# Kernel optimization log

Hardware: AMD Instinct MI355X
Metric: run time of the kernel (lower is better)

## Reference

```python
import jax, jax.numpy as jnp
import numpy as np

B, S, D, H, E = 8, 196, 768, 12, 8
HD = D // H  # 64
FF = 4 * D   # 3072
EPS = 1e-5


def setup_inputs() -> dict:
    key = jax.random.key(0)
    ks = jax.random.split(key, 12)
    s = 0.02
    inp = {
        'x': jax.random.normal(ks[0], (B, S, D), jnp.float32),
        'ln1_g': jnp.ones((D,), jnp.float32),
        'ln1_b': jnp.zeros((D,), jnp.float32),
        'Wq': jax.random.normal(ks[1], (D, D), jnp.float32) * s,
        'bq': jnp.zeros((D,), jnp.float32),
        'Wk': jax.random.normal(ks[2], (D, HD), jnp.float32) * s,
        'bk': jnp.zeros((HD,), jnp.float32),
        'Wv': jax.random.normal(ks[3], (D, HD), jnp.float32) * s,
        'bv': jnp.zeros((HD,), jnp.float32),
        'ln2_g': jnp.ones((D,), jnp.float32),
        'ln2_b': jnp.zeros((D,), jnp.float32),
        'Wg': jax.random.normal(ks[4], (D, E), jnp.float32) * s,
        'bg': jnp.zeros((E,), jnp.float32),
        'W1': jax.random.normal(ks[5], (E, D, FF), jnp.float32) * s,
        'b1': jnp.zeros((E, FF), jnp.float32),
        'W2': jax.random.normal(ks[6], (E, FF, D), jnp.float32) * s,
        'b2': jnp.zeros((E, D), jnp.float32),
    }
    return inp


def _layernorm(x, g, b):
    mu = jnp.mean(x, axis=-1, keepdims=True)
    var = jnp.var(x, axis=-1, keepdims=True)
    return (x - mu) * jax.lax.rsqrt(var + EPS) * g + b


def _rotate_half(x):
    x1, x2 = jnp.split(x, 2, axis=-1)
    return jnp.concatenate((-x2, x1), axis=-1)


def _rope(seq_len):
    inv_freq = 1.0 / (10000.0 ** (jnp.arange(0, HD, 2, dtype=jnp.float32) / HD))
    freqs = jnp.arange(seq_len, dtype=jnp.float32)[:, None] * inv_freq[None, :]
    emb = jnp.concatenate((freqs, freqs), axis=-1)  # [S, HD]
    return emb[None, :, None, :]  # [1, S, 1, HD]


def _attention(x, Wq, bq, Wk, bk, Wv, bv):
    b, s, _ = x.shape
    q = (x @ Wq + bq).reshape(b, s, H, HD)
    k = (x @ Wk + bk).reshape(b, s, 1, HD)
    v = (x @ Wv + bv).reshape(b, s, 1, HD)
    k = jnp.broadcast_to(k, (b, s, H, HD))
    v = jnp.broadcast_to(v, (b, s, H, HD))
    pe = _rope(s)
    cos, sin = jnp.cos(pe), jnp.sin(pe)
    q = q * cos + _rotate_half(q) * sin
    k = k * cos + _rotate_half(k) * sin
    scale = HD ** -0.5
    # NOTE: faithful to source -- matmul over the last two dims of [b,s,h,d],
    # i.e. attention across HEADS, not sequence positions.
    attn = jnp.einsum('bshd,bsgd->bshg', q, k) * scale
    attn = jax.nn.softmax(attn, axis=-1)
    out = jnp.einsum('bshg,bsgd->bshd', attn, v)
    return out.reshape(b, s, H * HD)


def _moe(x, Wg, bg, W1, b1, W2, b2):
    b, s, d = x.shape
    xt = x.reshape(-1, d)  # [T, D]
    gates = jax.nn.softmax(xt @ Wg + bg, axis=-1)
    top1 = jnp.argmax(gates, axis=-1)  # topk(k=2)[:,0] == argmax
    out = jnp.zeros_like(xt)
    for e in range(E):  # small fixed expert count
        h = jax.nn.gelu(xt @ W1[e] + b1[e], approximate=False)
        y = h @ W2[e] + b2[e]
        out = jnp.where((top1 == e)[:, None], y, out)
    return out.reshape(b, s, d)


def reference(x, ln1_g, ln1_b, Wq, bq, Wk, bk, Wv, bv, ln2_g, ln2_b, Wg, bg, W1, b1, W2, b2):
    res = x
    h = _layernorm(x, ln1_g, ln1_b)
    h = _attention(h, Wq, bq, Wk, bk, Wv, bv)
    x = res + h
    res = x
    h = _layernorm(x, ln2_g, ln2_b)
    h = _moe(h, Wg, bg, W1, b1, W2, b2)
    return res + h
```

## Files before the change

### kernel.cpp

```cpp
#include <hip/hip_runtime.h>


typedef unsigned short u16;
typedef short bf16x8_t __attribute__((ext_vector_type(8)));
typedef short bf16x4_t __attribute__((ext_vector_type(4)));
typedef float f32x4_t  __attribute__((ext_vector_type(4)));

#define T_TOK 1568
#define DM 768
#define HD 64
#define FF 3072
#define NE 8
#define LDSW 44

#define OFF_CNT   0
#define OFF_N12   32
#define OFF_ITEM1 64
#define OFF_ITEM2 864
#define OFF_BUCK  4096
#define OFF_H2    54272
#define OFF_HMID  2462720

__device__ __forceinline__ float bf2f(u16 h) {
    unsigned u = ((unsigned)h) << 16;
    return __builtin_bit_cast(float, u);
}
__device__ __forceinline__ u16 f2bf(float f) {
    unsigned u = __builtin_bit_cast(unsigned, f);
    unsigned r = (u + 0x7FFFu + ((u >> 16) & 1u)) >> 16;
    return (u16)r;
}
__device__ __forceinline__ float gelu_f(float x) {
    return 0.5f * x * (1.0f + erff(x * 0.70710678118654752440f));
}

__global__ __launch_bounds__(256) void k_pre(
        const float* __restrict__ x,
        const float* __restrict__ g1, const float* __restrict__ b1,
        const float* __restrict__ Wv, const float* __restrict__ bv,
        const float* __restrict__ g2, const float* __restrict__ b2g,
        const float* __restrict__ Wg, const float* __restrict__ bg,
        const float* __restrict__ b2moe,
        u16* __restrict__ h2, float* __restrict__ out,
        int* __restrict__ cnt, int* __restrict__ buck) {
    __shared__ __align__(16) u16 h1s[8 * DM];
    __shared__ float wgs[NE * DM];
    __shared__ float g2s[DM], b2s[DM];
    __shared__ float ps[4 * 8 * 64];
    __shared__ float vsm[8 * 64];
    int tid = threadIdx.x, lane = tid & 63, w = tid >> 6;
    int tb = blockIdx.x * 8;

    for (int idx = tid; idx < NE * DM; idx += 256) {
        int e = idx / DM, c = idx % DM;
        wgs[idx] = Wg[(size_t)c * NE + e];
    }
    for (int idx = tid; idx < DM; idx += 256) { g2s[idx] = g2[idx]; b2s[idx] = b2g[idx]; }

    float xv[2][12];
#pragma unroll
    for (int ttl = 0; ttl < 2; ttl++) {
        int tl = w * 2 + ttl;
        int t = tb + tl;
        const float* xp = x + (size_t)t * DM;
        float s = 0.0f;
#pragma unroll
        for (int i = 0; i < 12; i++) { float q = xp[lane + 64 * i]; xv[ttl][i] = q; s += q; }
#pragma unroll
        for (int m = 1; m < 64; m <<= 1) s += __shfl_xor(s, m);
        float mu = s * (1.0f / DM);
        float vs = 0.0f;
#pragma unroll
        for (int i = 0; i < 12; i++) { float d = xv[ttl][i] - mu; vs += d * d; }
#pragma unroll
        for (int m = 1; m < 64; m <<= 1) vs += __shfl_xor(vs, m);
        float rs = rsqrtf(vs * (1.0f / DM) + 1e-5f);
#pragma unroll
        for (int i = 0; i < 12; i++) {
            int c = lane + 64 * i;
            h1s[tl * DM + c] = f2bf((xv[ttl][i] - mu) * rs * g1[c] + b1[c]);
        }
    }
    __syncthreads();

    float acc[8];
#pragma unroll
    for (int tt = 0; tt < 8; tt++) acc[tt] = 0.0f;
    const float* wp = Wv + (size_t)(w * 192) * HD + lane;
    for (int kk = 0; kk < 192; kk += 4) {
        float w0 = wp[(size_t)(kk + 0) * HD];
        float w1 = wp[(size_t)(kk + 1) * HD];
        float w2 = wp[(size_t)(kk + 2) * HD];
        float w3 = wp[(size_t)(kk + 3) * HD];
        int kb = w * 192 + kk;
#pragma unroll
        for (int tt = 0; tt < 8; tt++) {
            bf16x4_t hh = *(const bf16x4_t*)&h1s[tt * DM + kb];
            acc[tt] += bf2f((u16)hh[0]) * w0 + bf2f((u16)hh[1]) * w1 +
                       bf2f((u16)hh[2]) * w2 + bf2f((u16)hh[3]) * w3;
        }
    }
#pragma unroll
    for (int tt = 0; tt < 8; tt++) ps[(w * 8 + tt) * 64 + lane] = acc[tt];
    __syncthreads();
#pragma unroll
    for (int s2 = 0; s2 < 2; s2++) {
        int tt = w * 2 + s2;
        vsm[tt * 64 + lane] = ps[tt * 64 + lane] + ps[(8 + tt) * 64 + lane] +
                              ps[(16 + tt) * 64 + lane] + ps[(24 + tt) * 64 + lane] +
                              bv[lane];
    }
    __syncthreads();

#pragma unroll
    for (int ttl = 0; ttl < 2; ttl++) {
        int tl = w * 2 + ttl;
        int t = tb + tl;
        float vl = vsm[tl * 64 + lane];
        float x2v[12];
        float s = 0.0f;
#pragma unroll
        for (int i = 0; i < 12; i++) { float q = xv[ttl][i] + vl; x2v[i] = q; s += q; }
#pragma unroll
        for (int m = 1; m < 64; m <<= 1) s += __shfl_xor(s, m);
        float mu = s * (1.0f / DM);
        float vs = 0.0f;
#pragma unroll
        for (int i = 0; i < 12; i++) { float d = x2v[i] - mu; vs += d * d; }
#pragma unroll
        for (int m = 1; m < 64; m <<= 1) vs += __shfl_xor(vs, m);
        float rs = rsqrtf(vs * (1.0f / DM) + 1e-5f);
        float le[NE];
#pragma unroll
        for (int e = 0; e < NE; e++) le[e] = 0.0f;
        u16* h2p = h2 + (size_t)t * DM;
#pragma unroll
        for (int i = 0; i < 12; i++) {
            int c = lane + 64 * i;
            float h = (x2v[i] - mu) * rs * g2s[c] + b2s[c];
            h2p[c] = f2bf(h);
#pragma unroll
            for (int e = 0; e < NE; e++) le[e] += h * wgs[e * DM + c];
        }
#pragma unroll
        for (int e = 0; e < NE; e++) {
#pragma unroll
            for (int m = 1; m < 64; m <<= 1) le[e] += __shfl_xor(le[e], m);
        }
        float best = le[0] + bg[0]; int be = 0;
#pragma unroll
        for (int e = 1; e < NE; e++) {
            float q = le[e] + bg[e];
            if (q > best) { best = q; be = e; }
        }
        if (lane == 0) {
            int pos = atomicAdd(&cnt[be], 1);
            buck[be * T_TOK + pos] = t;
        }
        float* op = out + (size_t)t * DM;
        const float* bp = b2moe + (size_t)be * DM;
#pragma unroll
        for (int i = 0; i < 12; i++) {
            int c = lane + 64 * i;
            op[c] = x2v[i] + bp[c];
        }
    }
}

__global__ void k_plan(const int* __restrict__ cnt, int* __restrict__ n12,
                       int* __restrict__ item1, int* __restrict__ item2) {
    if (threadIdx.x == 0) {
        int n1 = 0, n2 = 0;
        for (int e = 0; e < NE; e++) {
            int mts = (cnt[e] + 127) >> 7;
            for (int mt = 0; mt < mts; mt++) {
                int code = e * 64 + mt;
                item1[n1++] = code;
                for (int kc = 0; kc < 4; kc++) item2[n2++] = code * 4 + kc;
            }
        }
        n12[0] = n1; n12[1] = n2;
    }
}

__global__ __launch_bounds__(256) void k_moe_gemm1(
        const u16* __restrict__ h2, const float* __restrict__ W1,
        const float* __restrict__ b1, const int* __restrict__ cnt,
        const int* __restrict__ n12, const int* __restrict__ item1,
        const int* __restrict__ buck, u16* __restrict__ hmid) {
    int nt = blockIdx.x, n0 = nt * 128;
    int n1 = n12[0];
    int tid = threadIdx.x, lane = tid & 63, wid = tid >> 6;
    int arow = tid >> 2, ac = tid & 3;
    int bn = tid & 127, bkg = tid >> 7;
    int lr = lane & 15, q = lane >> 4;
    __shared__ __align__(16) u16 As[128 * LDSW];
    __shared__ __align__(16) u16 Bs[128 * LDSW];

    for (int it = blockIdx.y; it < n1; it += gridDim.y) {
        int code = item1[it];
        int e = code >> 6, mt = code & 63;
        int cnte = cnt[e], m0 = mt * 128;
        const float* W1e = W1 + (size_t)e * DM * FF;
        int atok[2];
#pragma unroll
        for (int j = 0; j < 2; j++) {
            int i = m0 + arow + 64 * j;
            atok[j] = (i < cnte) ? buck[e * T_TOK + i] : -1;
        }
        f32x4_t acc[2][8];
#pragma unroll
        for (int mi = 0; mi < 2; mi++)
#pragma unroll
            for (int ni = 0; ni < 8; ni++) acc[mi][ni] = (f32x4_t){0.f, 0.f, 0.f, 0.f};

        bf16x8_t a_pre[2];
        float b_pre[16];
#pragma unroll
        for (int j = 0; j < 2; j++) {
            bf16x8_t v = {0, 0, 0, 0, 0, 0, 0, 0};
            if (atok[j] >= 0) v = *(const bf16x8_t*)&h2[(size_t)atok[j] * DM + ac * 8];
            a_pre[j] = v;
        }
        {
            const float* bp = W1e + (size_t)(bkg * 16) * FF + n0 + bn;
#pragma unroll
            for (int kk = 0; kk < 16; kk++) b_pre[kk] = bp[(size_t)kk * FF];
        }
        const int NK = DM / 32;
        for (int kt = 0; kt < NK; kt++) {
            __syncthreads();
#pragma unroll
            for (int j = 0; j < 2; j++)
                *(bf16x8_t*)&As[(arow + 64 * j) * LDSW + ac * 8] = a_pre[j];
            {
                bf16x8_t p0, p1;
#pragma unroll
                for (int kk = 0; kk < 8; kk++) {
                    p0[kk] = (short)f2bf(b_pre[kk]);
                    p1[kk] = (short)f2bf(b_pre[kk + 8]);
                }
                *(bf16x8_t*)&Bs[bn * LDSW + bkg * 16] = p0;
                *(bf16x8_t*)&Bs[bn * LDSW + bkg * 16 + 8] = p1;
            }
            __syncthreads();
            if (kt + 1 < NK) {
                int k0 = (kt + 1) * 32;
#pragma unroll
                for (int j = 0; j < 2; j++) {
                    bf16x8_t v = {0, 0, 0, 0, 0, 0, 0, 0};
                    if (atok[j] >= 0)
                        v = *(const bf16x8_t*)&h2[(size_t)atok[j] * DM + k0 + ac * 8];
                    a_pre[j] = v;
                }
                const float* bp = W1e + (size_t)(k0 + bkg * 16) * FF + n0 + bn;
#pragma unroll
                for (int kk = 0; kk < 16; kk++) b_pre[kk] = bp[(size_t)kk * FF];
            }
            bf16x8_t af[2];
#pragma unroll
            for (int mi = 0; mi < 2; mi++)
                af[mi] = *(const bf16x8_t*)&As[(wid * 32 + mi * 16 + lr) * LDSW + q * 8];
#pragma unroll
            for (int ni = 0; ni < 8; ni++) {
                bf16x8_t bfr = *(const bf16x8_t*)&Bs[(ni * 16 + lr) * LDSW + q * 8];
#pragma unroll
                for (int mi = 0; mi < 2; mi++)
                    acc[mi][ni] = __builtin_amdgcn_mfma_f32_16x16x32_bf16(af[mi], bfr, acc[mi][ni], 0, 0, 0);
            }
        }
        float bias[8];
#pragma unroll
        for (int ni = 0; ni < 8; ni++) bias[ni] = b1[(size_t)e * FF + n0 + ni * 16 + lr];
#pragma unroll
        for (int mi = 0; mi < 2; mi++) {
#pragma unroll
            for (int r = 0; r < 4; r++) {
                int i = m0 + wid * 32 + mi * 16 + q * 4 + r;
                if (i < cnte) {
                    int t = buck[e * T_TOK + i];
                    size_t base = (size_t)t * FF + n0;
#pragma unroll
                    for (int ni = 0; ni < 8; ni++)
                        hmid[base + ni * 16 + lr] = f2bf(gelu_f(acc[mi][ni][r] + bias[ni]));
                }
            }
        }
    }
}

__global__ __launch_bounds__(256) void k_moe_gemm2(
        const u16* __restrict__ hmid, const float* __restrict__ W2,
        const int* __restrict__ cnt, const int* __restrict__ n12,
        const int* __restrict__ item2, const int* __restrict__ buck,
        float* __restrict__ out) {
    int nt = blockIdx.x, n0 = nt * 128;
    int n2 = n12[1];
    int tid = threadIdx.x, lane = tid & 63, wid = tid >> 6;
    int arow = tid >> 2, ac = tid & 3;
    int bn = tid & 127, bkg = tid >> 7;
    int lr = lane & 15, q = lane >> 4;
    __shared__ __align__(16) u16 As[128 * LDSW];
    __shared__ __align__(16) u16 Bs[128 * LDSW];

    for (int it = blockIdx.y; it < n2; it += gridDim.y) {
        int code2 = item2[it];
        int kc = code2 & 3, code = code2 >> 2;
        int e = code >> 6, mt = code & 63;
        int cnte = cnt[e], m0 = mt * 128;
        int kbase = kc * (FF / 4);
        const float* W2e = W2 + (size_t)e * FF * DM;
        int atok[2];
#pragma unroll
        for (int j = 0; j < 2; j++) {
            int i = m0 + arow + 64 * j;
            atok[j] = (i < cnte) ? buck[e * T_TOK + i] : -1;
        }
        f32x4_t acc[2][8];
#pragma unroll
        for (int mi = 0; mi < 2; mi++)
#pragma unroll
            for (int ni = 0; ni < 8; ni++) acc[mi][ni] = (f32x4_t){0.f, 0.f, 0.f, 0.f};

        bf16x8_t a_pre[2];
        float b_pre[16];
#pragma unroll
        for (int j = 0; j < 2; j++) {
            bf16x8_t v = {0, 0, 0, 0, 0, 0, 0, 0};
            if (atok[j] >= 0)
                v = *(const bf16x8_t*)&hmid[(size_t)atok[j] * FF + kbase + ac * 8];
            a_pre[j] = v;
        }
        {
            const float* bp = W2e + (size_t)(kbase + bkg * 16) * DM + n0 + bn;
#pragma unroll
            for (int kk = 0; kk < 16; kk++) b_pre[kk] = bp[(size_t)kk * DM];
        }
        const int NK = (FF / 4) / 32;
        for (int kt = 0; kt < NK; kt++) {
            __syncthreads();
#pragma unroll
            for (int j = 0; j < 2; j++)
                *(bf16x8_t*)&As[(arow + 64 * j) * LDSW + ac * 8] = a_pre[j];
            {
                bf16x8_t p0, p1;
#pragma unroll
                for (int kk = 0; kk < 8; kk++) {
                    p0[kk] = (short)f2bf(b_pre[kk]);
                    p1[kk] = (short)f2bf(b_pre[kk + 8]);
                }
                *(bf16x8_t*)&Bs[bn * LDSW + bkg * 16] = p0;
                *(bf16x8_t*)&Bs[bn * LDSW + bkg * 16 + 8] = p1;
            }
            __syncthreads();
            if (kt + 1 < NK) {
                int k0 = kbase + (kt + 1) * 32;
#pragma unroll
                for (int j = 0; j < 2; j++) {
                    bf16x8_t v = {0, 0, 0, 0, 0, 0, 0, 0};
                    if (atok[j] >= 0)
                        v = *(const bf16x8_t*)&hmid[(size_t)atok[j] * FF + k0 + ac * 8];
                    a_pre[j] = v;
                }
                const float* bp = W2e + (size_t)(k0 + bkg * 16) * DM + n0 + bn;
#pragma unroll
                for (int kk = 0; kk < 16; kk++) b_pre[kk] = bp[(size_t)kk * DM];
            }
            bf16x8_t af[2];
#pragma unroll
            for (int mi = 0; mi < 2; mi++)
                af[mi] = *(const bf16x8_t*)&As[(wid * 32 + mi * 16 + lr) * LDSW + q * 8];
#pragma unroll
            for (int ni = 0; ni < 8; ni++) {
                bf16x8_t bfr = *(const bf16x8_t*)&Bs[(ni * 16 + lr) * LDSW + q * 8];
#pragma unroll
                for (int mi = 0; mi < 2; mi++)
                    acc[mi][ni] = __builtin_amdgcn_mfma_f32_16x16x32_bf16(af[mi], bfr, acc[mi][ni], 0, 0, 0);
            }
        }
#pragma unroll
        for (int mi = 0; mi < 2; mi++) {
#pragma unroll
            for (int r = 0; r < 4; r++) {
                int i = m0 + wid * 32 + mi * 16 + q * 4 + r;
                if (i < cnte) {
                    int t = buck[e * T_TOK + i];
                    size_t base = (size_t)t * DM + n0;
#pragma unroll
                    for (int ni = 0; ni < 8; ni++)
                        atomicAdd(&out[base + ni * 16 + lr], acc[mi][ni][r]);
                }
            }
        }
    }
}

extern "C" void kernel_launch(void* const* d_in, const int* in_sizes, int n_in,
                              void* d_out, int out_size, void* d_ws, size_t ws_size,
                              hipStream_t stream) {
    const float* x    = (const float*)d_in[0];
    const float* ln1g = (const float*)d_in[1];
    const float* ln1b = (const float*)d_in[2];
    const float* Wv   = (const float*)d_in[7];
    const float* bv   = (const float*)d_in[8];
    const float* ln2g = (const float*)d_in[9];
    const float* ln2b = (const float*)d_in[10];
    const float* Wg   = (const float*)d_in[11];
    const float* bg   = (const float*)d_in[12];
    const float* W1   = (const float*)d_in[13];
    const float* b1   = (const float*)d_in[14];
    const float* W2   = (const float*)d_in[15];
    const float* b2   = (const float*)d_in[16];

    char* ws = (char*)d_ws;
    int*   cnt   = (int*)(ws + OFF_CNT);
    int*   n12   = (int*)(ws + OFF_N12);
    int*   item1 = (int*)(ws + OFF_ITEM1);
    int*   item2 = (int*)(ws + OFF_ITEM2);
    int*   buck  = (int*)(ws + OFF_BUCK);
    u16*   h2    = (u16*)(ws + OFF_H2);
    u16*   hmid  = (u16*)(ws + OFF_HMID);
    float* out   = (float*)d_out;

    hipMemsetAsync(cnt, 0, 16 * sizeof(int), stream);
    k_pre<<<T_TOK / 8, 256, 0, stream>>>(x, ln1g, ln1b, Wv, bv, ln2g, ln2b,
                                         Wg, bg, b2, h2, out, cnt, buck);
    k_plan<<<1, 64, 0, stream>>>(cnt, n12, item1, item2);
    k_moe_gemm1<<<dim3(FF / 128, 24), 256, 0, stream>>>(h2, W1, b1, cnt, n12,
                                                        item1, buck, hmid);
    k_moe_gemm2<<<dim3(DM / 128, 96), 256, 0, stream>>>(hmid, W2, cnt, n12,
                                                        item2, buck, out);
}
```

Before: 322.6 us.

## Pre-transpose expert weights to bf16, use static grids and deterministic split-K reduction

Adds a kernel that converts W1 and W2 to bf16 and transposes them to N-major order on every call. The expert GEMMs can then load B tiles with 16-byte vector reads instead of strided fp32 loads with per-element conversion. The GEMMs now use a BK=64 tile, and the persistent work-list plan kernel is replaced by a static grid with early exit for empty tiles. The split-K atomics in gemm2 are replaced by partial buffers plus a separate reduce kernel. The weight transpose reads all fp32 weights and writes bf16 copies each call, which adds memory traffic and two extra launches in exchange for cheaper GEMM inner loops.

```diff
diff --git a/kernel.cpp b/kernel.cpp
--- a/kernel.cpp
+++ b/kernel.cpp
@@ -11,15 +11,15 @@
 #define HD 64
 #define FF 3072
 #define NE 8
-#define LDSW 44
+#define MT_MAX 13
 
 #define OFF_CNT   0
-#define OFF_N12   32
-#define OFF_ITEM1 64
-#define OFF_ITEM2 864
-#define OFF_BUCK  4096
-#define OFF_H2    54272
-#define OFF_HMID  2462720
+#define OFF_BUCK  64
+#define OFF_H2    50304
+#define OFF_HMID  2458752
+#define OFF_W1T   12092544
+#define OFF_W2T   49841280
+#define OFF_PART  87590016
 
 __device__ __forceinline__ float bf2f(u16 h) {
     unsigned u = ((unsigned)h) << 16;
@@ -32,6 +32,49 @@
 }
 __device__ __forceinline__ float gelu_f(float x) {
     return 0.5f * x * (1.0f + erff(x * 0.70710678118654752440f));
+}
+
+__global__ __launch_bounds__(256) void k_wt(const float* __restrict__ W1,
+                                            const float* __restrict__ W2,
+                                            u16* __restrict__ W1t,
+                                            u16* __restrict__ W2t) {
+    __shared__ __align__(16) u16 Ls[64 * 68];
+    int z = blockIdx.z;
+    const float* src;
+    u16* dst;
+    int K, N, k0, n0;
+    if (z < 8) {
+        src = W1 + (size_t)z * DM * FF;
+        dst = W1t + (size_t)z * DM * FF;
+        K = DM; N = FF;
+        n0 = blockIdx.x * 64; k0 = blockIdx.y * 64;
+    } else {
+        src = W2 + (size_t)(z - 8) * FF * DM;
+        dst = W2t + (size_t)(z - 8) * FF * DM;
+        K = FF; N = DM;
+        k0 = blockIdx.x * 64; n0 = blockIdx.y * 64;
+    }
+    int tid = threadIdx.x;
+#pragma unroll
+    for (int j = 0; j < 4; j++) {
+        int cid = tid + 256 * j;
+        int r = cid >> 4, c4 = cid & 15;
+        f32x4_t v = *(const f32x4_t*)&src[(size_t)(k0 + r) * N + n0 + c4 * 4];
+        bf16x4_t h;
+        h[0] = (short)f2bf(v[0]); h[1] = (short)f2bf(v[1]);
+        h[2] = (short)f2bf(v[2]); h[3] = (short)f2bf(v[3]);
+        *(bf16x4_t*)&Ls[r * 68 + c4 * 4] = h;
+    }
+    __syncthreads();
+#pragma unroll
+    for (int j = 0; j < 2; j++) {
+        int cid = tid + 256 * j;
+        int n = cid >> 3, c = cid & 7;
+        bf16x8_t o;
+#pragma unroll
+        for (int kk = 0; kk < 8; kk++) o[kk] = (short)Ls[(c * 8 + kk) * 68 + n];
+        *(bf16x8_t*)&dst[(size_t)(n0 + n) * K + k0 + c * 8] = o;
+    }
 }
 
 __global__ __launch_bounds__(256) void k_pre(
@@ -167,231 +210,221 @@
     }
 }
 
-__global__ void k_plan(const int* __restrict__ cnt, int* __restrict__ n12,
-                       int* __restrict__ item1, int* __restrict__ item2) {
-    if (threadIdx.x == 0) {
-        int n1 = 0, n2 = 0;
-        for (int e = 0; e < NE; e++) {
-            int mts = (cnt[e] + 127) >> 7;
-            for (int mt = 0; mt < mts; mt++) {
-                int code = e * 64 + mt;
-                item1[n1++] = code;
-                for (int kc = 0; kc < 4; kc++) item2[n2++] = code * 4 + kc;
-            }
-        }
-        n12[0] = n1; n12[1] = n2;
-    }
-}
-
 __global__ __launch_bounds__(256) void k_moe_gemm1(
-        const u16* __restrict__ h2, const float* __restrict__ W1,
+        const u16* __restrict__ h2, const u16* __restrict__ W1t,
         const float* __restrict__ b1, const int* __restrict__ cnt,
-        const int* __restrict__ n12, const int* __restrict__ item1,
         const int* __restrict__ buck, u16* __restrict__ hmid) {
-    int nt = blockIdx.x, n0 = nt * 128;
-    int n1 = n12[0];
+    int e = blockIdx.y / MT_MAX, mt = blockIdx.y % MT_MAX;
+    int cnte = cnt[e];
+    int m0 = mt * 128;
+    if (m0 >= cnte) return;
+    int n0 = blockIdx.x * 128;
+    const u16* Bw = W1t + (size_t)e * DM * FF;
+    __shared__ __align__(16) u16 As[128 * 72];
+    __shared__ __align__(16) u16 Bs[128 * 72];
     int tid = threadIdx.x, lane = tid & 63, wid = tid >> 6;
-    int arow = tid >> 2, ac = tid & 3;
-    int bn = tid & 127, bkg = tid >> 7;
+    int srow = tid >> 3, sc = tid & 7;
     int lr = lane & 15, q = lane >> 4;
-    __shared__ __align__(16) u16 As[128 * LDSW];
-    __shared__ __align__(16) u16 Bs[128 * LDSW];
-
-    for (int it = blockIdx.y; it < n1; it += gridDim.y) {
-        int code = item1[it];
-        int e = code >> 6, mt = code & 63;
-        int cnte = cnt[e], m0 = mt * 128;
-        const float* W1e = W1 + (size_t)e * DM * FF;
-        int atok[2];
-#pragma unroll
-        for (int j = 0; j < 2; j++) {
-            int i = m0 + arow + 64 * j;
-            atok[j] = (i < cnte) ? buck[e * T_TOK + i] : -1;
-        }
-        f32x4_t acc[2][8];
-#pragma unroll
-        for (int mi = 0; mi < 2; mi++)
-#pragma unroll
-            for (int ni = 0; ni < 8; ni++) acc[mi][ni] = (f32x4_t){0.f, 0.f, 0.f, 0.f};
-
-        bf16x8_t a_pre[2];
-        float b_pre[16];
-#pragma unroll
-        for (int j = 0; j < 2; j++) {
-            bf16x8_t v = {0, 0, 0, 0, 0, 0, 0, 0};
-            if (atok[j] >= 0) v = *(const bf16x8_t*)&h2[(size_t)atok[j] * DM + ac * 8];
-            a_pre[j] = v;
-        }
-        {
-            const float* bp = W1e + (size_t)(bkg * 16) * FF + n0 + bn;
-#pragma unroll
-            for (int kk = 0; kk < 16; kk++) b_pre[kk] = bp[(size_t)kk * FF];
-        }
-        const int NK = DM / 32;
-        for (int kt = 0; kt < NK; kt++) {
-            __syncthreads();
-#pragma unroll
-            for (int j = 0; j < 2; j++)
-                *(bf16x8_t*)&As[(arow + 64 * j) * LDSW + ac * 8] = a_pre[j];
-            {
-                bf16x8_t p0, p1;
-#pragma unroll
-                for (int kk = 0; kk < 8; kk++) {
-                    p0[kk] = (short)f2bf(b_pre[kk]);
-                    p1[kk] = (short)f2bf(b_pre[kk + 8]);
-                }
-                *(bf16x8_t*)&Bs[bn * LDSW + bkg * 16] = p0;
-                *(bf16x8_t*)&Bs[bn * LDSW + bkg * 16 + 8] = p1;
-            }
-            __syncthreads();
-            if (kt + 1 < NK) {
-                int k0 = (kt + 1) * 32;
-#pragma unroll
-                for (int j = 0; j < 2; j++) {
-                    bf16x8_t v = {0, 0, 0, 0, 0, 0, 0, 0};
-                    if (atok[j] >= 0)
-                        v = *(const bf16x8_t*)&h2[(size_t)atok[j] * DM + k0 + ac * 8];
-                    a_pre[j] = v;
-                }
-                const float* bp = W1e + (size_t)(k0 + bkg * 16) * FF + n0 + bn;
-#pragma unroll
-                for (int kk = 0; kk < 16; kk++) b_pre[kk] = bp[(size_t)kk * FF];
-            }
+
+    int atok[4];
+#pragma unroll
+    for (int j = 0; j < 4; j++) {
+        int i = m0 + srow + 32 * j;
+        atok[j] = (i < cnte) ? buck[e * T_TOK + i] : -1;
+    }
+    f32x4_t acc[2][8];
+#pragma unroll
+    for (int mi = 0; mi < 2; mi++)
+#pragma unroll
+        for (int ni = 0; ni < 8; ni++) acc[mi][ni] = (f32x4_t){0.f, 0.f, 0.f, 0.f};
+
+    bf16x8_t a_pre[4], b_pre[4];
+#pragma unroll
+    for (int j = 0; j < 4; j++) {
+        bf16x8_t v = {0, 0, 0, 0, 0, 0, 0, 0};
+        if (atok[j] >= 0) v = *(const bf16x8_t*)&h2[(size_t)atok[j] * DM + sc * 8];
+        a_pre[j] = v;
+        b_pre[j] = *(const bf16x8_t*)&Bw[(size_t)(n0 + srow + 32 * j) * DM + sc * 8];
+    }
+    const int NK = DM / 64;
+    for (int kt = 0; kt < NK; kt++) {
+        __syncthreads();
+#pragma unroll
+        for (int j = 0; j < 4; j++) {
+            *(bf16x8_t*)&As[(srow + 32 * j) * 72 + sc * 8] = a_pre[j];
+            *(bf16x8_t*)&Bs[(srow + 32 * j) * 72 + sc * 8] = b_pre[j];
+        }
+        __syncthreads();
+        if (kt + 1 < NK) {
+            int k0 = (kt + 1) * 64;
+#pragma unroll
+            for (int j = 0; j < 4; j++) {
+                bf16x8_t v = {0, 0, 0, 0, 0, 0, 0, 0};
+                if (atok[j] >= 0)
+                    v = *(const bf16x8_t*)&h2[(size_t)atok[j] * DM + k0 + sc * 8];
+                a_pre[j] = v;
+                b_pre[j] = *(const bf16x8_t*)&Bw[(size_t)(n0 + srow + 32 * j) * DM + k0 + sc * 8];
+            }
+        }
+#pragma unroll
+        for (int s = 0; s < 2; s++) {
             bf16x8_t af[2];
 #pragma unroll
             for (int mi = 0; mi < 2; mi++)
-                af[mi] = *(const bf16x8_t*)&As[(wid * 32 + mi * 16 + lr) * LDSW + q * 8];
+                af[mi] = *(const bf16x8_t*)&As[(wid * 32 + mi * 16 + lr) * 72 + s * 32 + q * 8];
 #pragma unroll
             for (int ni = 0; ni < 8; ni++) {
-                bf16x8_t bfr = *(const bf16x8_t*)&Bs[(ni * 16 + lr) * LDSW + q * 8];
+                bf16x8_t bfr = *(const bf16x8_t*)&Bs[(ni * 16 + lr) * 72 + s * 32 + q * 8];
 #pragma unroll
                 for (int mi = 0; mi < 2; mi++)
                     acc[mi][ni] = __builtin_amdgcn_mfma_f32_16x16x32_bf16(af[mi], bfr, acc[mi][ni], 0, 0, 0);
             }
         }
-        float bias[8];
-#pragma unroll
-        for (int ni = 0; ni < 8; ni++) bias[ni] = b1[(size_t)e * FF + n0 + ni * 16 + lr];
-#pragma unroll
-        for (int mi = 0; mi < 2; mi++) {
-#pragma unroll
-            for (int r = 0; r < 4; r++) {
-                int i = m0 + wid * 32 + mi * 16 + q * 4 + r;
-                if (i < cnte) {
-                    int t = buck[e * T_TOK + i];
-                    size_t base = (size_t)t * FF + n0;
-#pragma unroll
-                    for (int ni = 0; ni < 8; ni++)
-                        hmid[base + ni * 16 + lr] = f2bf(gelu_f(acc[mi][ni][r] + bias[ni]));
-                }
+    }
+    float bias[8];
+#pragma unroll
+    for (int ni = 0; ni < 8; ni++) bias[ni] = b1[(size_t)e * FF + n0 + ni * 16 + lr];
+#pragma unroll
+    for (int mi = 0; mi < 2; mi++) {
+#pragma unroll
+        for (int r = 0; r < 4; r++) {
+            int i = m0 + wid * 32 + mi * 16 + q * 4 + r;
+            if (i < cnte) {
+                int t = buck[e * T_TOK + i];
+                size_t base = (size_t)t * FF + n0;
+#pragma unroll
+                for (int ni = 0; ni < 8; ni++)
+                    hmid[base + ni * 16 + lr] = f2bf(gelu_f(acc[mi][ni][r] + bias[ni]));
             }
         }
     }
 }
 
 __global__ __launch_bounds__(256) void k_moe_gemm2(
-        const u16* __restrict__ hmid, const float* __restrict__ W2,
-        const int* __restrict__ cnt, const int* __restrict__ n12,
-        const int* __restrict__ item2, const int* __restrict__ buck,
-        float* __restrict__ out) {
-    int nt = blockIdx.x, n0 = nt * 128;
-    int n2 = n12[1];
+        const u16* __restrict__ hmid, const u16* __restrict__ W2t,
+        const int* __restrict__ cnt, const int* __restrict__ buck,
+        float* __restrict__ part) {
+    int y = blockIdx.y;
+    int e = y / (MT_MAX * 4);
+    int rem = y % (MT_MAX * 4);
+    int mt = rem >> 2, kc = rem & 3;
+    int cnte = cnt[e];
+    int m0 = mt * 128;
+    if (m0 >= cnte) return;
+    int n0 = blockIdx.x * 128;
+    int kbase = kc * (FF / 4);
+    int off = 0;
+    for (int ee = 0; ee < NE; ee++) off += (ee < e) ? cnt[ee] : 0;
+    const u16* Bw = W2t + (size_t)e * DM * FF;
+    __shared__ __align__(16) u16 As[128 * 72];
+    __shared__ __align__(16) u16 Bs[128 * 72];
     int tid = threadIdx.x, lane = tid & 63, wid = tid >> 6;
-    int arow = tid >> 2, ac = tid & 3;
-    int bn = tid & 127, bkg = tid >> 7;
+    int srow = tid >> 3, sc = tid & 7;
     int lr = lane & 15, q = lane >> 4;
-    __shared__ __align__(16) u16 As[128 * LDSW];
-    __shared__ __align__(16) u16 Bs[128 * LDSW];
-
-    for (int it = blockIdx.y; it < n2; it += gridDim.y) {
-        int code2 = item2[it];
-        int kc = code2 & 3, code = code2 >> 2;
-        int e = code >> 6, mt = code & 63;
-        int cnte = cnt[e], m0 = mt * 128;
-        int kbase = kc * (FF / 4);
-        const float* W2e = W2 + (size_t)e * FF * DM;
-        int atok[2];
-#pragma unroll
-        for (int j = 0; j < 2; j++) {
-            int i = m0 + arow + 64 * j;
-            atok[j] = (i < cnte) ? buck[e * T_TOK + i] : -1;
-        }
-        f32x4_t acc[2][8];
-#pragma unroll
-        for (int mi = 0; mi < 2; mi++)
-#pragma unroll
-            for (int ni = 0; ni < 8; ni++) acc[mi][ni] = (f32x4_t){0.f, 0.f, 0.f, 0.f};
-
-        bf16x8_t a_pre[2];
-        float b_pre[16];
-#pragma unroll
-        for (int j = 0; j < 2; j++) {
-            bf16x8_t v = {0, 0, 0, 0, 0, 0, 0, 0};
-            if (atok[j] >= 0)
-                v = *(const bf16x8_t*)&hmid[(size_t)atok[j] * FF + kbase + ac * 8];
-            a_pre[j] = v;
-        }
-        {
-            const float* bp = W2e + (size_t)(kbase + bkg * 16) * DM + n0 + bn;
-#pragma unroll
-            for (int kk = 0; kk < 16; kk++) b_pre[kk] = bp[(size_t)kk * DM];
-        }
-        const int NK = (FF / 4) / 32;
-        for (int kt = 0; kt < NK; kt++) {
-            __syncthreads();
-#pragma unroll
-            for (int j = 0; j < 2; j++)
-                *(bf16x8_t*)&As[(arow + 64 * j) * LDSW + ac * 8] = a_pre[j];
-            {
-                bf16x8_t p0, p1;
-#pragma unroll
-                for (int kk = 0; kk < 8; kk++) {
-                    p0[kk] = (short)f2bf(b_pre[kk]);
-                    p1[kk] = (short)f2bf(b_pre[kk + 8]);
-                }
-                *(bf16x8_t*)&Bs[bn * LDSW + bkg * 16] = p0;
-                *(bf16x8_t*)&Bs[bn * LDSW + bkg * 16 + 8] = p1;
-            }
-            __syncthreads();
-            if (kt + 1 < NK) {
-                int k0 = kbase + (kt + 1) * 32;
-#pragma unroll
-                for (int j = 0; j < 2; j++) {
-                    bf16x8_t v = {0, 0, 0, 0, 0, 0, 0, 0};
-                    if (atok[j] >= 0)
-                        v = *(const bf16x8_t*)&hmid[(size_t)atok[j] * FF + k0 + ac * 8];
-                    a_pre[j] = v;
-                }
-                const float* bp = W2e + (size_t)(k0 + bkg * 16) * DM + n0 + bn;
-#pragma unroll
-                for (int kk = 0; kk < 16; kk++) b_pre[kk] = bp[(size_t)kk * DM];
-            }
+
+    int atok[4];
+#pragma unroll
+    for (int j = 0; j < 4; j++) {
+        int i = m0 + srow + 32 * j;
+        atok[j] = (i < cnte) ? buck[e * T_TOK + i] : -1;
+    }
+    f32x4_t acc[2][8];
+#pragma unroll
+    for (int mi = 0; mi < 2; mi++)
+#pragma unroll
+        for (int ni = 0; ni < 8; ni++) acc[mi][ni] = (f32x4_t){0.f, 0.f, 0.f, 0.f};
+
+    bf16x8_t a_pre[4], b_pre[4];
+#pragma unroll
+    for (int j = 0; j < 4; j++) {
+        bf16x8_t v = {0, 0, 0, 0, 0, 0, 0, 0};
+        if (atok[j] >= 0)
+            v = *(const bf16x8_t*)&hmid[(size_t)atok[j] * FF + kbase + sc * 8];
+        a_pre[j] = v;
+        b_pre[j] = *(const bf16x8_t*)&Bw[(size_t)(n0 + srow + 32 * j) * FF + kbase + sc * 8];
+    }
+    const int NK = (FF / 4) / 64;
+    for (int kt = 0; kt < NK; kt++) {
+        __syncthreads();
+#pragma unroll
+        for (int j = 0; j < 4; j++) {
+            *(bf16x8_t*)&As[(srow + 32 * j) * 72 + sc * 8] = a_pre[j];
+            *(bf16x8_t*)&Bs[(srow + 32 * j) * 72 + sc * 8] = b_pre[j];
+        }
+        __syncthreads();
+        if (kt + 1 < NK) {
+            int k0 = kbase + (kt + 1) * 64;
+#pragma unroll
+            for (int j = 0; j < 4; j++) {
+                bf16x8_t v = {0, 0, 0, 0, 0, 0, 0, 0};
+                if (atok[j] >= 0)
+                    v = *(const bf16x8_t*)&hmid[(size_t)atok[j] * FF + k0 + sc * 8];
+                a_pre[j] = v;
+                b_pre[j] = *(const bf16x8_t*)&Bw[(size_t)(n0 + srow + 32 * j) * FF + k0 + sc * 8];
+            }
+        }
+#pragma unroll
+        for (int s = 0; s < 2; s++) {
             bf16x8_t af[2];
 #pragma unroll
             for (int mi = 0; mi < 2; mi++)
-                af[mi] = *(const bf16x8_t*)&As[(wid * 32 + mi * 16 + lr) * LDSW + q * 8];
+                af[mi] = *(const bf16x8_t*)&As[(wid * 32 + mi * 16 + lr) * 72 + s * 32 + q * 8];
 #pragma unroll
             for (int ni = 0; ni < 8; ni++) {
-                bf16x8_t bfr = *(const bf16x8_t*)&Bs[(ni * 16 + lr) * LDSW + q * 8];
+                bf16x8_t bfr = *(const bf16x8_t*)&Bs[(ni * 16 + lr) * 72 + s * 32 + q * 8];
 #pragma unroll
                 for (int mi = 0; mi < 2; mi++)
                     acc[mi][ni] = __builtin_amdgcn_mfma_f32_16x16x32_bf16(af[mi], bfr, acc[mi][ni], 0, 0, 0);
             }
         }
-#pragma unroll
-        for (int mi = 0; mi < 2; mi++) {
-#pragma unroll
-            for (int r = 0; r < 4; r++) {
-                int i = m0 + wid * 32 + mi * 16 + q * 4 + r;
-                if (i < cnte) {
-                    int t = buck[e * T_TOK + i];
-                    size_t base = (size_t)t * DM + n0;
-#pragma unroll
-                    for (int ni = 0; ni < 8; ni++)
-                        atomicAdd(&out[base + ni * 16 + lr], acc[mi][ni][r]);
-                }
-            }
-        }
+    }
+    float* pbase = part + (size_t)kc * T_TOK * DM;
+#pragma unroll
+    for (int mi = 0; mi < 2; mi++) {
+#pragma unroll
+        for (int r = 0; r < 4; r++) {
+            int i = m0 + wid * 32 + mi * 16 + q * 4 + r;
+            if (i < cnte) {
+                float* pp = pbase + (size_t)(off + i) * DM + n0;
+#pragma unroll
+                for (int ni = 0; ni < 8; ni++)
+                    pp[ni * 16 + lr] = acc[mi][ni][r];
+            }
+        }
+    }
+}
+
+__global__ __launch_bounds__(256) void k_reduce(
+        const float* __restrict__ part, const int* __restrict__ cnt,
+        const int* __restrict__ buck, float* __restrict__ out) {
+    int y = blockIdx.y;
+    int e = y / MT_MAX, mt = y % MT_MAX;
+    int cnte = cnt[e];
+    int m0 = mt * 128;
+    if (m0 >= cnte) return;
+    int off = 0;
+    for (int ee = 0; ee < NE; ee++) off += (ee < e) ? cnt[ee] : 0;
+    int n0 = blockIdx.x * 128;
+    int tid = threadIdx.x;
+    int rl = tid >> 1, half = tid & 1;
+    int i = m0 + rl;
+    if (i >= cnte) return;
+    int t = buck[e * T_TOK + i];
+    int g = off + i;
+    size_t colb = (size_t)n0 + half * 64;
+    const float* p0 = part + (size_t)0 * T_TOK * DM + (size_t)g * DM + colb;
+    const float* p1 = part + (size_t)1 * T_TOK * DM + (size_t)g * DM + colb;
+    const float* p2 = part + (size_t)2 * T_TOK * DM + (size_t)g * DM + colb;
+    const float* p3 = part + (size_t)3 * T_TOK * DM + (size_t)g * DM + colb;
+    float* op = out + (size_t)t * DM + colb;
+#pragma unroll
+    for (int v = 0; v < 16; v++) {
+        f32x4_t s = *(const f32x4_t*)&p0[v * 4];
+        s += *(const f32x4_t*)&p1[v * 4];
+        s += *(const f32x4_t*)&p2[v * 4];
+        s += *(const f32x4_t*)&p3[v * 4];
+        f32x4_t o = *(const f32x4_t*)&op[v * 4];
+        *(f32x4_t*)&op[v * 4] = o + s;
     }
 }
 
@@ -413,21 +446,22 @@
     const float* b2   = (const float*)d_in[16];
 
     char* ws = (char*)d_ws;
-    int*   cnt   = (int*)(ws + OFF_CNT);
-    int*   n12   = (int*)(ws + OFF_N12);
-    int*   item1 = (int*)(ws + OFF_ITEM1);
-    int*   item2 = (int*)(ws + OFF_ITEM2);
-    int*   buck  = (int*)(ws + OFF_BUCK);
-    u16*   h2    = (u16*)(ws + OFF_H2);
-    u16*   hmid  = (u16*)(ws + OFF_HMID);
-    float* out   = (float*)d_out;
+    int*   cnt  = (int*)(ws + OFF_CNT);
+    int*   buck = (int*)(ws + OFF_BUCK);
+    u16*   h2   = (u16*)(ws + OFF_H2);
+    u16*   hmid = (u16*)(ws + OFF_HMID);
+    u16*   W1t  = (u16*)(ws + OFF_W1T);
+    u16*   W2t  = (u16*)(ws + OFF_W2T);
+    float* part = (float*)(ws + OFF_PART);
+    float* out  = (float*)d_out;
 
     hipMemsetAsync(cnt, 0, 16 * sizeof(int), stream);
+    k_wt<<<dim3(48, 12, 16), 256, 0, stream>>>(W1, W2, W1t, W2t);
     k_pre<<<T_TOK / 8, 256, 0, stream>>>(x, ln1g, ln1b, Wv, bv, ln2g, ln2b,
                                          Wg, bg, b2, h2, out, cnt, buck);
-    k_plan<<<1, 64, 0, stream>>>(cnt, n12, item1, item2);
-    k_moe_gemm1<<<dim3(FF / 128, 24), 256, 0, stream>>>(h2, W1, b1, cnt, n12,
-                                                        item1, buck, hmid);
-    k_moe_gemm2<<<dim3(DM / 128, 96), 256, 0, stream>>>(hmid, W2, cnt, n12,
-                                                        item2, buck, out);
-}
+    k_moe_gemm1<<<dim3(FF / 128, NE * MT_MAX), 256, 0, stream>>>(
+        h2, W1t, b1, cnt, buck, hmid);
+    k_moe_gemm2<<<dim3(DM / 128, NE * MT_MAX * 4), 256, 0, stream>>>(
+        hmid, W2t, cnt, buck, part);
+    k_reduce<<<dim3(DM / 128, NE * MT_MAX), 256, 0, stream>>>(part, cnt, buck, out);
+}
```

New measurement: 347.9 us. 1.08x slower.
